# Kernel optimization log

Hardware: AMD Instinct MI355X
Metric: run time of the kernel (lower is better)

The kernel has to match this reference:

```python
import jax, jax.numpy as jnp
import numpy as np

H = 8   # num_heads
D = 64  # out_features per head

def setup_inputs() -> dict:
    key = jax.random.key(0)
    k1, k2, k3, k4 = jax.random.split(key, 4)
    B, N, F_IN, E = 2, 8192, 512, 65536
    x = jax.random.normal(k1, (B, N, F_IN), dtype=jnp.float32)
    edge_indices = jax.random.randint(k2, (2, E), 0, N)
    W = jax.random.normal(k3, (H * D, F_IN), dtype=jnp.float32) * (1.0 / np.sqrt(F_IN))
    a = jax.random.normal(k4, (2 * D, 1), dtype=jnp.float32) * 0.1
    return {"x": x, "edge_indices": edge_indices, "W": W, "a": a}

def reference(x, edge_indices, W, a):
    # Faithful translation of GraphAttentionLayer.forward (eval mode: dropout = identity).
    B, N, _ = x.shape
    h = (x @ W.T).reshape(B, N, H, D)              # [B,N,H,D]
    src, dst = edge_indices[0], edge_indices[1]
    E = src.shape[0]
    h_src = h[:, src]                               # [B,E,H,D]
    h_dst = h[:, dst]                               # [B,E,H,D]
    # cat([h_src,h_dst]) @ a  ==  h_src @ a[:D] + h_dst @ a[D:]
    a1, a2 = a[:D, 0], a[D:, 0]
    scores = jnp.einsum('behd,d->beh', h_src, a1) + jnp.einsum('behd,d->beh', h_dst, a2)
    scores = jax.nn.leaky_relu(scores, negative_slope=0.2)      # [B,E,H]
    # NOTE: original code softmaxes over the BATCH dim (dim=0) per edge.
    sm = jax.nn.softmax(scores, axis=0)                          # [B,E,H]
    last_edge = jnp.full((N,), -1, dtype=jnp.int32).at[src].max(
        jnp.arange(E, dtype=jnp.int32))                          # [N]
    has_edge = last_edge >= 0
    w = jnp.where(has_edge[None, :, None],
                  sm[:, jnp.clip(last_edge, 0)], 0.0)            # [B,N,H]
    # aggregated[:, s] += w[:, s, :, None] * h_dst[:, e] for each edge e with src[e]==s
    # (weights fully built before aggregation loop) => w[s] * segment_sum(h_dst over src)
    agg_dst = jnp.zeros((B, N, H, D), dtype=h.dtype).at[:, src].add(h_dst)
    aggregated = w[..., None] * agg_dst                          # [B,N,H,D]
    return aggregated.mean(axis=2)                               # [B,N,D]
```

## Files before the change

kernel.cpp:

```cpp
#include <hip/hip_runtime.h>
#include <stdint.h>

#define H_HEADS 8
#define DDIM 64
#define NNODES 8192
#define BB 2
#define FIN 512
#define FOUT 512
#define EDGES 65536
#define CAP 32

typedef unsigned short u16;
typedef unsigned int u32;
typedef __bf16 bf16x8 __attribute__((ext_vector_type(8)));
typedef float f32x4 __attribute__((ext_vector_type(4)));

__device__ __forceinline__ u16 f2bf(float f) {
    u32 u = __float_as_uint(f);
    return (u16)((u + 0x7FFFu + ((u >> 16) & 1u)) >> 16);
}
__device__ __forceinline__ float bf2f(u32 s) {
    return __uint_as_float(s << 16);
}
__device__ __forceinline__ uint4 pack8(float4 a, float4 b) {
    return make_uint4(f2bf(a.x) | ((u32)f2bf(a.y) << 16),
                      f2bf(a.z) | ((u32)f2bf(a.w) << 16),
                      f2bf(b.x) | ((u32)f2bf(b.y) << 16),
                      f2bf(b.z) | ((u32)f2bf(b.w) << 16));
}

#define NEB 64
#define NWB (FOUT * FIN / 8 / 256)
#define NXB (BB * NNODES * FIN / 8 / 256)
__global__ __launch_bounds__(256) void prep_kernel(
    const float* __restrict__ W, const float* __restrict__ X,
    const int* __restrict__ src, const int* __restrict__ dst,
    u16* __restrict__ Wb, u16* __restrict__ Xb,
    int* __restrict__ cursor, int* __restrict__ le_pack,
    int* __restrict__ csr_dst) {
    int blk = blockIdx.x;
    if (blk < NEB) {
        int t = blk * 256 + threadIdx.x;
#pragma unroll
        for (int k = 0; k < 4; k++) {
            int e = t * 4 + k;
            int s = src[e], d = dst[e];
            int slot = atomicAdd(&cursor[s], 1);
            if (slot < CAP) csr_dst[(size_t)s * CAP + slot] = d;
            atomicMax(&le_pack[s], (e << 13) | d);
        }
    } else if (blk < NEB + NWB) {
        int i = (blk - NEB) * 256 + threadIdx.x;
        const float4* p = (const float4*)W;
        float4 v0 = p[(size_t)i * 2], v1 = p[(size_t)i * 2 + 1];
        ((uint4*)Wb)[i] = pack8(v0, v1);
    } else {
        int i = (blk - NEB - NWB) * 256 + threadIdx.x;
        const float4* p = (const float4*)X;
        float4 v0 = p[(size_t)i * 2], v1 = p[(size_t)i * 2 + 1];
        ((uint4*)Xb)[i] = pack8(v0, v1);
    }
}

#define GLDS(g, l)                                                              \
    __builtin_amdgcn_global_load_lds(                                           \
        (const __attribute__((address_space(1))) u32*)(g),                      \
        (__attribute__((address_space(3))) u32*)(l), 16, 0, 0)

__global__ __launch_bounds__(256) void gemm_mfma(const u16* __restrict__ Am,
                                                 const u16* __restrict__ Bm,
                                                 const float* __restrict__ a,
                                                 u16* __restrict__ C,
                                                 float* __restrict__ s1,
                                                 float* __restrict__ s2) {
    __shared__ u16 As[128 * 32];
    __shared__ u16 Bs[128 * 32];
    int tid = threadIdx.x;
    int gb = blockIdx.x;
    int m_idx = (gb & 7) | ((gb >> 5) << 3);
    int n_idx = (gb >> 3) & 3;
    int m0 = m_idx * 128, n0 = n_idx * 128;
    int lane = tid & 63, wv = tid >> 6;
    int wr = (wv >> 1) * 64, wc = (wv & 1) * 64;
    int l15 = lane & 15, quad = lane >> 4;
    f32x4 acc[4][4] = {};

    float a1v[4], a2v[4];
#pragma unroll
    for (int j = 0; j < 4; j++) {
        a1v[j] = a[j * 16 + l15];
        a2v[j] = a[DDIM + j * 16 + l15];
    }

    int srow = tid >> 2;
    int scol = (tid & 3) * 8;
    const u16* Ag = Am + (size_t)(m0 + srow) * FIN + scol;
    const u16* Bg = Bm + (size_t)(n0 + srow) * FIN + scol;
    u16* Al = As + tid * 8;
    u16* Bl = Bs + tid * 8;

    for (int k0 = 0; k0 < FIN; k0 += 32) {
        __syncthreads();
        GLDS(Ag + k0, Al);
        GLDS(Ag + k0 + (size_t)64 * FIN, Al + 64 * 32);
        GLDS(Bg + k0, Bl);
        GLDS(Bg + k0 + (size_t)64 * FIN, Bl + 64 * 32);
        __syncthreads();
        bf16x8 af[4], bfr[4];
#pragma unroll
        for (int i = 0; i < 4; i++)
            af[i] = *(const bf16x8*)(As + (wr + i * 16 + l15) * 32 + quad * 8);
#pragma unroll
        for (int j = 0; j < 4; j++)
            bfr[j] = *(const bf16x8*)(Bs + (wc + j * 16 + l15) * 32 + quad * 8);
#pragma unroll
        for (int i = 0; i < 4; i++)
#pragma unroll
            for (int j = 0; j < 4; j++)
                acc[i][j] = __builtin_amdgcn_mfma_f32_16x16x32_bf16(
                    af[i], bfr[j], acc[i][j], 0, 0, 0);
    }

#pragma unroll
    for (int i = 0; i < 4; i++) {
        int row_base = m0 + wr + i * 16 + quad * 4;
#pragma unroll
        for (int j = 0; j < 4; j++) {
            int col = n0 + wc + j * 16 + l15;
#pragma unroll
            for (int r = 0; r < 4; r++)
                C[(size_t)(row_base + r) * FOUT + col] = f2bf(acc[i][j][r]);
        }
    }

    int head = n_idx * 2 + (wv & 1);
#pragma unroll
    for (int i = 0; i < 4; i++) {
#pragma unroll
        for (int r = 0; r < 4; r++) {
            float p1 = 0.f, p2 = 0.f;
#pragma unroll
            for (int j = 0; j < 4; j++) {
                p1 += a1v[j] * acc[i][j][r];
                p2 += a2v[j] * acc[i][j][r];
            }
#pragma unroll
            for (int m = 1; m <= 8; m <<= 1) {
                p1 += __shfl_xor(p1, m);
                p2 += __shfl_xor(p2, m);
            }
            if (l15 == 0) {
                int row = m0 + wr + i * 16 + quad * 4 + r;
                s1[row * H_HEADS + head] = p1;
                s2[row * H_HEADS + head] = p2;
            }
        }
    }
}

__device__ __forceinline__ void acc8(float* acc, uint4 v) {
    acc[0] += bf2f(v.x & 0xffffu);
    acc[1] += bf2f(v.x >> 16);
    acc[2] += bf2f(v.y & 0xffffu);
    acc[3] += bf2f(v.y >> 16);
    acc[4] += bf2f(v.z & 0xffffu);
    acc[5] += bf2f(v.z >> 16);
    acc[6] += bf2f(v.w & 0xffffu);
    acc[7] += bf2f(v.w >> 16);
}

__global__ __launch_bounds__(256) void aggregate(const u16* __restrict__ h,
                                                 const float* __restrict__ s1,
                                                 const float* __restrict__ s2,
                                                 const int* __restrict__ cursor,
                                                 const int* __restrict__ le_pack,
                                                 const int* __restrict__ csr_dst,
                                                 float* __restrict__ out, int N) {
    int n = blockIdx.x * 2 + (threadIdx.x >> 7);
    int b = (threadIdx.x >> 6) & 1;
    int lane = threadIdx.x & 63;
    int head = lane >> 3;

    int deg = cursor[n];
    deg = deg < CAP ? deg : CAP;
    int pk = le_pack[n];

    const int* cp = csr_dst + (size_t)n * CAP;
    int myidx = (lane < CAP) ? cp[lane] : 0;

    float wgt = 0.f;
    if (deg > 0) {
        int dl = pk & 8191;
        float sc0 = s1[(0 * N + n) * H_HEADS + head] +
                    s2[((size_t)0 * N + dl) * H_HEADS + head];
        float sc1 = s1[((size_t)1 * N + n) * H_HEADS + head] +
                    s2[((size_t)1 * N + dl) * H_HEADS + head];
        sc0 = sc0 >= 0.f ? sc0 : 0.2f * sc0;
        sc1 = sc1 >= 0.f ? sc1 : 0.2f * sc1;
        float m = fmaxf(sc0, sc1);
        float e0 = __expf(sc0 - m), e1 = __expf(sc1 - m);
        wgt = (b == 0 ? e0 : e1) / (e0 + e1);
    }

    float acc[8] = {};
    const u16* hb = h + (size_t)b * N * FOUT + lane * 8;
    int degm = deg & ~3;
    for (int j0 = 0; j0 < degm; j0 += 4) {
        int d0 = __shfl(myidx, j0);
        int d1 = __shfl(myidx, j0 + 1);
        int d2 = __shfl(myidx, j0 + 2);
        int d3 = __shfl(myidx, j0 + 3);
        uint4 v0 = *(const uint4*)(hb + (size_t)d0 * FOUT);
        uint4 v1 = *(const uint4*)(hb + (size_t)d1 * FOUT);
        uint4 v2 = *(const uint4*)(hb + (size_t)d2 * FOUT);
        uint4 v3 = *(const uint4*)(hb + (size_t)d3 * FOUT);
        acc8(acc, v0);
        acc8(acc, v1);
        acc8(acc, v2);
        acc8(acc, v3);
    }
    for (int j = degm; j < deg; j++) {
        int dn = __shfl(myidx, j);
        uint4 v = *(const uint4*)(hb + (size_t)dn * FOUT);
        acc8(acc, v);
    }

    float val[8];
#pragma unroll
    for (int k = 0; k < 8; k++) val[k] = acc[k] * wgt;
#pragma unroll
    for (int m = 8; m <= 32; m <<= 1)
#pragma unroll
        for (int k = 0; k < 8; k++) val[k] += __shfl_xor(val[k], m);
    if (lane < 8) {
        float* op = out + ((size_t)b * N + n) * DDIM + lane * 8;
        const float inv = 1.0f / H_HEADS;
        *(float4*)op = make_float4(val[0] * inv, val[1] * inv, val[2] * inv,
                                   val[3] * inv);
        *(float4*)(op + 4) = make_float4(val[4] * inv, val[5] * inv,
                                         val[6] * inv, val[7] * inv);
    }
}

extern "C" void kernel_launch(void* const* d_in, const int* in_sizes, int n_in,
                              void* d_out, int out_size, void* d_ws,
                              size_t ws_size, hipStream_t stream) {
    const float* x = (const float*)d_in[0];
    const int* edges = (const int*)d_in[1];
    const float* W = (const float*)d_in[2];
    const float* a = (const float*)d_in[3];
    float* out = (float*)d_out;

    const int* src = edges;
    const int* dst = edges + EDGES;

    char* p = (char*)d_ws;
    auto carve = [&](size_t bytes) {
        char* r = p;
        p += (bytes + 255) & ~(size_t)255;
        return r;
    };
    u16* Wb = (u16*)carve((size_t)FOUT * FIN * 2);
    u16* Xb = (u16*)carve((size_t)BB * NNODES * FIN * 2);
    u16* h = (u16*)carve((size_t)BB * NNODES * FOUT * 2);
    float* s1 = (float*)carve((size_t)BB * NNODES * H_HEADS * 4);
    float* s2 = (float*)carve((size_t)BB * NNODES * H_HEADS * 4);
    int* cursor = (int*)carve(NNODES * 4);
    int* le_pack = (int*)carve(NNODES * 4);
    int* csr_dst = (int*)carve((size_t)NNODES * CAP * 4);

    const int M = BB * NNODES;

    hipMemsetAsync(cursor, 0, 2 * NNODES * 4, stream);
    prep_kernel<<<NEB + NWB + NXB, 256, 0, stream>>>(W, x, src, dst, Wb, Xb,
                                                     cursor, le_pack, csr_dst);
    gemm_mfma<<<(M / 128) * (FOUT / 128), 256, 0, stream>>>(Xb, Wb, a, h, s1,
                                                            s2);
    aggregate<<<NNODES / 2, 256, 0, stream>>>(h, s1, s2, cursor, le_pack,
                                              csr_dst, out, NNODES);
}
```

Baseline: 126.3 us.

## Triple-buffer GEMM LDS tiles with async global_load_lds prefetch

Converts the single-buffered K loop of the projection GEMM into a three-stage ring of LDS buffers. Loads for tile t+2 are issued before computing tile t, with explicit vmcnt waits and barriers, so global memory latency overlaps with MFMA work. LDS use triples and the manual wait counts must match the number of outstanding loads. Loading of the attention vector is also moved after the main loop to ease register pressure.

```diff
diff --git a/kernel.cpp b/kernel.cpp
--- a/kernel.cpp
+++ b/kernel.cpp
@@ -73,8 +73,8 @@
                                                  u16* __restrict__ C,
                                                  float* __restrict__ s1,
                                                  float* __restrict__ s2) {
-    __shared__ u16 As[128 * 32];
-    __shared__ u16 Bs[128 * 32];
+    __shared__ u16 As[3][128 * 32];
+    __shared__ u16 Bs[3][128 * 32];
     int tid = threadIdx.x;
     int gb = blockIdx.x;
     int m_idx = (gb & 7) | ((gb >> 5) << 3);
@@ -85,41 +85,55 @@
     int l15 = lane & 15, quad = lane >> 4;
     f32x4 acc[4][4] = {};
 
-    float a1v[4], a2v[4];
-#pragma unroll
-    for (int j = 0; j < 4; j++) {
-        a1v[j] = a[j * 16 + l15];
-        a2v[j] = a[DDIM + j * 16 + l15];
-    }
-
     int srow = tid >> 2;
     int scol = (tid & 3) * 8;
     const u16* Ag = Am + (size_t)(m0 + srow) * FIN + scol;
     const u16* Bg = Bm + (size_t)(n0 + srow) * FIN + scol;
-    u16* Al = As + tid * 8;
-    u16* Bl = Bs + tid * 8;
-
-    for (int k0 = 0; k0 < FIN; k0 += 32) {
-        __syncthreads();
-        GLDS(Ag + k0, Al);
-        GLDS(Ag + k0 + (size_t)64 * FIN, Al + 64 * 32);
-        GLDS(Bg + k0, Bl);
-        GLDS(Bg + k0 + (size_t)64 * FIN, Bl + 64 * 32);
-        __syncthreads();
-        bf16x8 af[4], bfr[4];
-#pragma unroll
-        for (int i = 0; i < 4; i++)
-            af[i] = *(const bf16x8*)(As + (wr + i * 16 + l15) * 32 + quad * 8);
-#pragma unroll
-        for (int j = 0; j < 4; j++)
-            bfr[j] = *(const bf16x8*)(Bs + (wc + j * 16 + l15) * 32 + quad * 8);
-#pragma unroll
-        for (int i = 0; i < 4; i++)
-#pragma unroll
-            for (int j = 0; j < 4; j++)
-                acc[i][j] = __builtin_amdgcn_mfma_f32_16x16x32_bf16(
-                    af[i], bfr[j], acc[i][j], 0, 0, 0);
-    }
+
+#define STAGE(c, kk)                                                            \
+    do {                                                                        \
+        u16* Al_ = As[c] + tid * 8;                                             \
+        u16* Bl_ = Bs[c] + tid * 8;                                             \
+        GLDS(Ag + (kk), Al_);                                                   \
+        GLDS(Ag + (kk) + (size_t)64 * FIN, Al_ + 64 * 32);                      \
+        GLDS(Bg + (kk), Bl_);                                                   \
+        GLDS(Bg + (kk) + (size_t)64 * FIN, Bl_ + 64 * 32);                      \
+    } while (0)
+
+#define COMPUTE(c)                                                              \
+    do {                                                                        \
+        bf16x8 af[4], bfr[4];                                                   \
+        _Pragma("unroll") for (int i = 0; i < 4; i++) af[i] =                   \
+            *(const bf16x8*)(As[c] + (wr + i * 16 + l15) * 32 + quad * 8);      \
+        _Pragma("unroll") for (int j = 0; j < 4; j++) bfr[j] =                  \
+            *(const bf16x8*)(Bs[c] + (wc + j * 16 + l15) * 32 + quad * 8);      \
+        _Pragma("unroll") for (int i = 0; i < 4; i++)                           \
+            _Pragma("unroll") for (int j = 0; j < 4; j++) acc[i][j] =           \
+                __builtin_amdgcn_mfma_f32_16x16x32_bf16(af[i], bfr[j],          \
+                                                        acc[i][j], 0, 0, 0);    \
+    } while (0)
+
+    STAGE(0, 0);
+    STAGE(1, 32);
+    int c0 = 0, c2 = 2;
+#pragma unroll 1
+    for (int t = 0; t < 14; ++t) {
+        asm volatile("s_waitcnt vmcnt(4)" ::: "memory");
+        __builtin_amdgcn_s_barrier();
+        __builtin_amdgcn_sched_barrier(0);
+        STAGE(c2, (t + 2) * 32);
+        COMPUTE(c0);
+        c0 = (c0 == 2) ? 0 : c0 + 1;
+        c2 = (c2 == 2) ? 0 : c2 + 1;
+    }
+    asm volatile("s_waitcnt vmcnt(4)" ::: "memory");
+    __builtin_amdgcn_s_barrier();
+    __builtin_amdgcn_sched_barrier(0);
+    COMPUTE(2);
+    asm volatile("s_waitcnt vmcnt(0)" ::: "memory");
+    __builtin_amdgcn_s_barrier();
+    __builtin_amdgcn_sched_barrier(0);
+    COMPUTE(0);
 
 #pragma unroll
     for (int i = 0; i < 4; i++) {
@@ -133,6 +147,12 @@
         }
     }
 
+    float a1v[4], a2v[4];
+#pragma unroll
+    for (int j = 0; j < 4; j++) {
+        a1v[j] = a[j * 16 + l15];
+        a2v[j] = a[DDIM + j * 16 + l15];
+    }
     int head = n_idx * 2 + (wv & 1);
 #pragma unroll
     for (int i = 0; i < 4; i++) {
```

Result: no change. 125.6 us (-0.5%).
